# Kernel tuning notes

Hardware: AMD Instinct MI355X
Metric: run time of the kernel (lower is better)

Reference implementation:

```python
import jax, jax.numpy as jnp
import numpy as np

ADAPTER_RATIO = 0.2


def setup_inputs() -> dict:
    key = jax.random.key(0)
    k1, k2, k3, k4, k5 = jax.random.split(key, 5)
    B, C, H, D = 16384, 512, 128, 3  # batch, feature dim, bottleneck, n_domains
    n_text = (D + 1) * 345           # original + 3 domain prompt sets, 345 classes
    return {
        "image_features": jax.random.normal(k1, (B, C), dtype=jnp.float32),
        "domain_label": jax.random.randint(k2, (B,), 0, D),
        "W1": jax.random.normal(k3, (D, C, H), dtype=jnp.float32) * 0.02,
        "W2": jax.random.normal(k4, (D, H, C), dtype=jnp.float32) * 0.02,
        "text_features": jax.random.normal(k5, (n_text, C), dtype=jnp.float32),
        "logit_scale": jnp.ones((1,), dtype=jnp.float32) * jnp.log(jnp.float32(100.0)),
    }


def reference(image_features, domain_label, W1, W2, text_features, logit_scale):
    # Per-sample routed adapters: run all D tiny adapters densely, then gather
    # each sample's routed output (equivalent to torch per-sample dispatch loop).
    h = jax.nn.relu(jnp.einsum("bi,dij->dbj", image_features, W1))   # [D,B,H]
    a = jax.nn.relu(jnp.einsum("dbj,djk->dbk", h, W2))                # [D,B,C]
    adapter_features = jnp.take_along_axis(
        a, domain_label[None, :, None], axis=0)[0]                     # [B,C]
    feats = ADAPTER_RATIO * adapter_features + (1.0 - ADAPTER_RATIO) * image_features
    feats = feats / jnp.linalg.norm(feats, axis=-1, keepdims=True)
    # text features are pre-normalized in the original module
    txt = text_features / jnp.linalg.norm(text_features, axis=-1, keepdims=True)
    logits = jnp.exp(logit_scale[0]) * (feats @ txt.T)                 # [B, n_text]
    return logits
```

## Files before the change

kernel.cpp:

```cpp
#include <hip/hip_runtime.h>
#include <math.h>

typedef __bf16 bf16;
typedef __attribute__((ext_vector_type(8))) __bf16 bf16x8;
typedef __attribute__((ext_vector_type(4))) __bf16 bf16x4;
typedef __attribute__((ext_vector_type(4))) float f32x4;

#define MFMA(a, b, c) __builtin_amdgcn_mfma_f32_16x16x32_bf16((a), (b), (c), 0, 0, 0)
#define BARR() __builtin_amdgcn_s_barrier()
#define SFEN() __builtin_amdgcn_sched_barrier(0)
#define WAITV(n) asm volatile("s_waitcnt vmcnt(" #n ")" ::: "memory")
#define LGKM0() asm volatile("s_waitcnt lgkmcnt(0)" ::: "memory")

static constexpr int NB = 16384;
static constexpr int NC = 512;
static constexpr int NH = 128;
static constexpr int ND = 3;
static constexpr int NT = 1380;
static constexpr int NTP = 1408;
static constexpr int NTILE = 131;
static constexpr int NPMAX = NTILE * 128;

__device__ __forceinline__ void gld16(const bf16* g, void* l) {
  __builtin_amdgcn_global_load_lds(
      (const __attribute__((address_space(1))) void*)g,
      (__attribute__((address_space(3))) void*)l, 16, 0, 0);
}

__global__ __launch_bounds__(1024) void k_prep(
    const float* __restrict__ W1, const float* __restrict__ W2,
    const float* __restrict__ txt, const int* __restrict__ lab,
    bf16* __restrict__ W1t, bf16* __restrict__ W2t, bf16* __restrict__ Tbf,
    int* __restrict__ map, int* __restrict__ dmeta)
{
  __shared__ float tl[64][65];
  __shared__ int woff[16][3];
  __shared__ int segbase[4];
  __shared__ int padded[3];
  const int b = blockIdx.x, t = threadIdx.x;

  if (b < 88) {
    const int wv = t >> 6, lane = t & 63;
    const int row = b * 16 + wv;
    bf16x4* dst = (bf16x4*)(Tbf + (size_t)row * NC);
    if (row < NT) {
      const float4* src = (const float4*)(txt + (size_t)row * NC);
      float4 u0 = src[lane * 2], u1 = src[lane * 2 + 1];
      float ssq = u0.x * u0.x + u0.y * u0.y + u0.z * u0.z + u0.w * u0.w +
                  u1.x * u1.x + u1.y * u1.y + u1.z * u1.z + u1.w * u1.w;
      for (int m = 32; m; m >>= 1) ssq += __shfl_xor(ssq, m, 64);
      float inv = 1.0f / sqrtf(ssq);
      bf16x4 o0 = {(bf16)(u0.x * inv), (bf16)(u0.y * inv), (bf16)(u0.z * inv), (bf16)(u0.w * inv)};
      bf16x4 o1 = {(bf16)(u1.x * inv), (bf16)(u1.y * inv), (bf16)(u1.z * inv), (bf16)(u1.w * inv)};
      dst[lane * 2] = o0; dst[lane * 2 + 1] = o1;
    } else {
      bf16x4 z = {(bf16)0.f, (bf16)0.f, (bf16)0.f, (bf16)0.f};
      dst[lane * 2] = z; dst[lane * 2 + 1] = z;
    }
  } else if (b < 136) {
    const int e = b - 88, d = e >> 4, rem = e & 15;
    const int i0 = (rem >> 1) * 64, n0 = (rem & 1) * 64;
    const int rr = t >> 4, c4 = (t & 15) * 4;
    const float* src = W1 + (size_t)d * NC * NH;
    float4 v = *(const float4*)&src[(size_t)(i0 + rr) * NH + n0 + c4];
    tl[rr][c4] = v.x; tl[rr][c4 + 1] = v.y; tl[rr][c4 + 2] = v.z; tl[rr][c4 + 3] = v.w;
    __syncthreads();
    bf16* dst = W1t + (size_t)d * NH * NC;
    bf16x4 o = {(bf16)tl[c4][rr], (bf16)tl[c4 + 1][rr],
                (bf16)tl[c4 + 2][rr], (bf16)tl[c4 + 3][rr]};
    *(bf16x4*)&dst[(size_t)(n0 + rr) * NC + i0 + c4] = o;
  } else if (b < 184) {
    const int e = b - 136, d = e >> 4, rem = e & 15;
    const int j0 = (rem >> 3) * 64, n0 = (rem & 7) * 64;
    const int rr = t >> 4, c4 = (t & 15) * 4;
    const float* src = W2 + (size_t)d * NH * NC;
    float4 v = *(const float4*)&src[(size_t)(j0 + rr) * NC + n0 + c4];
    tl[rr][c4] = v.x; tl[rr][c4 + 1] = v.y; tl[rr][c4 + 2] = v.z; tl[rr][c4 + 3] = v.w;
    __syncthreads();
    bf16* dst = W2t + (size_t)d * NC * NH;
    bf16x4 o = {(bf16)tl[c4][rr], (bf16)tl[c4 + 1][rr],
                (bf16)tl[c4 + 2][rr], (bf16)tl[c4 + 3][rr]};
    *(bf16x4*)&dst[(size_t)(n0 + rr) * NH + j0 + c4] = o;
  } else {
    const int lane = t & 63, wv = t >> 6;
    int c[3] = {0, 0, 0};
    int ld[16];
    const int base = t * 16;
#pragma unroll
    for (int i = 0; i < 16; ++i) { ld[i] = lab[base + i]; c[ld[i]]++; }
    int exc[3];
#pragma unroll
    for (int d = 0; d < 3; ++d) {
      int v = c[d];
      for (int off = 1; off < 64; off <<= 1) {
        int u = __shfl_up(v, off, 64);
        if (lane >= off) v += u;
      }
      exc[d] = v - c[d];
      if (lane == 63) woff[wv][d] = v;
    }
    __syncthreads();
    if (t == 0) {
      int tot[3] = {0, 0, 0};
      for (int w = 0; w < 16; ++w)
        for (int d = 0; d < 3; ++d) { int v = woff[w][d]; woff[w][d] = tot[d]; tot[d] += v; }
      int s = 0;
      for (int d = 0; d < 3; ++d) {
        padded[d] = (tot[d] + 127) & ~127;
        segbase[d] = s; s += padded[d];
      }
      segbase[3] = s;
      dmeta[NTILE] = s;
    }
    __syncthreads();
    for (int tile = t; tile < NTILE; tile += 1024) {
      const int slot = tile * 128;
      int dd = -1;
      for (int d = 0; d < 3; ++d)
        if (slot >= segbase[d] && slot < segbase[d] + padded[d]) dd = d;
      dmeta[tile] = dd;
    }
    for (int i = t; i < NPMAX; i += 1024) map[i] = -1;
    __syncthreads();
    int pos[3];
#pragma unroll
    for (int d = 0; d < 3; ++d) pos[d] = segbase[d] + woff[wv][d] + exc[d];
#pragma unroll
    for (int i = 0; i < 16; ++i) { int d = ld[i]; map[pos[d]++] = base + i; }
  }
}

__global__ __launch_bounds__(512) void k_adapter(
    const float* __restrict__ X, const bf16* __restrict__ W1t,
    const bf16* __restrict__ W2t, const int* __restrict__ map,
    const int* __restrict__ dmeta, bf16* __restrict__ Fbf)
{
  __shared__ bf16 As[8][64 * 64];
  __shared__ bf16 Hs[64 * 128];
  __shared__ float rssq[8][64];
  __shared__ int smap[64];
  const int bx = blockIdx.x;
  const int d = dmeta[bx >> 1];
  if (d < 0) return;
  const int t = threadIdx.x, w = t >> 6, l = t & 63;
  const int lr = l & 15, lg = l >> 4;
  const int row0 = bx * 64;
  if (t < 64) smap[t] = map[row0 + t];

  int arow = map[row0 + (t >> 3)]; if (arow < 0) arow = 0;
  const float4* Xr = (const float4*)(X + (size_t)arow * NC);
  const int f4b = (t & 7) * 2;
  const int wrow = t >> 3;
  const int wcb = ((t & 7) * 16) ^ ((wrow & 7) << 4);

  float4 R0a, R0b, R1a, R1b;
#define LOADR0(kt) { R0a = Xr[(kt) * 16 + f4b]; R0b = Xr[(kt) * 16 + f4b + 1]; }
#define LOADR1(kt) { R1a = Xr[(kt) * 16 + f4b]; R1b = Xr[(kt) * 16 + f4b + 1]; }
#define CVTW(kt, Ra, Rb) {                                                    \
    bf16x8 v_;                                                                \
    v_[0] = (bf16)Ra.x; v_[1] = (bf16)Ra.y; v_[2] = (bf16)Ra.z;               \
    v_[3] = (bf16)Ra.w; v_[4] = (bf16)Rb.x; v_[5] = (bf16)Rb.y;               \
    v_[6] = (bf16)Rb.z; v_[7] = (bf16)Rb.w;                                   \
    *(bf16x8*)((char*)As[kt] + wrow * 128 + wcb) = v_; }

  f32x4 acc1[4] = {};
  const bf16* W1B = W1t + (size_t)d * NH * NC + (size_t)(w * 16 + lr) * NC;
  LOADR0(0); LOADR1(1);
  CVTW(0, R0a, R0b);
  LOADR0(2);
  LGKM0(); BARR(); SFEN();
#pragma unroll 1
  for (int kt = 0; kt < 8; ++kt) {
    if (kt + 1 < 8) {
      if ((kt & 1) == 0) { CVTW(kt + 1, R1a, R1b); if (kt + 3 < 8) LOADR1(kt + 3); }
      else              { CVTW(kt + 1, R0a, R0b); if (kt + 3 < 8) LOADR0(kt + 3); }
    }
#pragma unroll
    for (int h = 0; h < 2; ++h) {
      bf16x8 a[4];
#pragma unroll
      for (int m = 0; m < 4; ++m) {
        const int r = m * 16 + lr;
        a[m] = *(const bf16x8*)((const char*)As[kt] +
                                r * 128 + ((h * 64 + lg * 16) ^ ((r & 7) << 4)));
      }
      const bf16x8 bq = *(const bf16x8*)(W1B + kt * 64 + h * 32 + lg * 8);
#pragma unroll
      for (int m = 0; m < 4; ++m) acc1[m] = MFMA(a[m], bq, acc1[m]);
    }
    LGKM0(); SFEN(); BARR(); SFEN();
  }
#undef LOADR0
#undef LOADR1
#undef CVTW

#pragma unroll
  for (int m = 0; m < 4; ++m)
#pragma unroll
    for (int r = 0; r < 4; ++r) {
      const int row = m * 16 + lg * 4 + r;
      const int colb = (w * 16 + lr) * 2;
      const float v = acc1[m][r];
      *(bf16*)((char*)Hs + row * 256 + (colb ^ ((row & 7) << 4))) =
          (bf16)(v > 0.f ? v : 0.f);
    }
  __syncthreads();

  f32x4 acc[4][4] = {};
  const bf16* W2B = W2t + (size_t)d * NC * NH + (size_t)(w * 64) * NH;
#pragma unroll
  for (int ks = 0; ks < 4; ++ks) {
    bf16x8 a[4], bq[4];
#pragma unroll
    for (int m = 0; m < 4; ++m) {
      const int r = m * 16 + lr;
      a[m] = *(const bf16x8*)((const char*)Hs +
                              r * 256 + ((ks * 64 + lg * 16) ^ ((r & 7) << 4)));
    }
#pragma unroll
    for (int n = 0; n < 4; ++n)
      bq[n] = *(const bf16x8*)(W2B + (size_t)(n * 16 + lr) * NH + ks * 32 + lg * 8);
#pragma unroll
    for (int m = 0; m < 4; ++m)
#pragma unroll
      for (int n = 0; n < 4; ++n)
        acc[m][n] = MFMA(a[m], bq[n], acc[m][n]);
  }

  const int col0 = w * 64;
#pragma unroll
  for (int m = 0; m < 4; ++m)
#pragma unroll
    for (int r = 0; r < 4; ++r) {
      const int rl = m * 16 + lg * 4 + r;
      const int grow = smap[rl];
      float part = 0.f;
#pragma unroll
      for (int n = 0; n < 4; ++n) {
        const int cw = n * 16 + lr;
        const float xv = (float)*(const bf16*)((const char*)As[w] +
                              rl * 128 + ((cw * 2) ^ ((rl & 7) << 4)));
        float v = acc[m][n][r];
        v = v > 0.f ? v : 0.f;
        v = 0.2f * v + 0.8f * xv;
        acc[m][n][r] = v;
        part += v * v;
      }
      part += __shfl_xor(part, 1, 64);
      part += __shfl_xor(part, 2, 64);
      part += __shfl_xor(part, 4, 64);
      part += __shfl_xor(part, 8, 64);
      if (lr == 0) rssq[w][rl] = part;
      (void)grow;
    }
  __syncthreads();
#pragma unroll
  for (int m = 0; m < 4; ++m)
#pragma unroll
    for (int r = 0; r < 4; ++r) {
      const int rl = m * 16 + lg * 4 + r;
      const int grow = smap[rl];
      if (grow < 0) continue;
      float tot = 0.f;
#pragma unroll
      for (int ww = 0; ww < 8; ++ww) tot += rssq[ww][rl];
      const float inv = 1.0f / sqrtf(tot);
#pragma unroll
      for (int n = 0; n < 4; ++n) {
        const int col = col0 + n * 16 + lr;
        Fbf[(size_t)grow * NC + col] = (bf16)(acc[m][n][r] * inv);
      }
    }
}

__global__ __launch_bounds__(256) void k_gemm3(
    const bf16* __restrict__ Fbf, const bf16* __restrict__ Tbf,
    const float* __restrict__ lsc, float* __restrict__ out)
{
  __shared__ bf16 As[2][128 * 32];
  __shared__ bf16 Bs[2][128 * 32];
  const int bx = blockIdx.x, by = blockIdx.y;
  const int t = threadIdx.x, w = t >> 6, l = t & 63;
  const int wr = w >> 1, wc = w & 1;
  const int lr = l & 15, lg = l >> 4;
  const int row0 = bx * 128, col0 = by * 128;
  const bf16* Ag = Fbf + (size_t)row0 * NC;
  const bf16* Bg = Tbf + (size_t)col0 * NC;

#define STG3(buf, kt)                                                         \
  {                                                                           \
    _Pragma("unroll")                                                         \
    for (int i = 0; i < 2; ++i) {                                             \
      const int off = (i * 256 + t) * 16;                                     \
      const int row = off >> 6;                                               \
      const int src = (off & 63) ^ (((row >> 1) & 3) << 4);                   \
      const size_t go = (size_t)row * NC + (size_t)(kt) * 32 + (src >> 1);    \
      gld16(Ag + go, (char*)As[buf] + off);                                   \
      gld16(Bg + go, (char*)Bs[buf] + off);                                   \
    }                                                                         \
  }

  f32x4 acc[4][4] = {};
  STG3(0, 0);
#pragma unroll 1
  for (int ks = 0; ks < 16; ++ks) {
    const int cur = ks & 1;
    __syncthreads();
    if (ks + 1 < 16) STG3(cur ^ 1, ks + 1);
    bf16x8 a[4], b[4];
#pragma unroll
    for (int m = 0; m < 4; ++m) {
      const int r = wr * 64 + m * 16 + lr;
      a[m] = *(const bf16x8*)&As[cur][r * 32 + ((lg * 8) ^ (((r >> 1) & 3) << 3))];
    }
#pragma unroll
    for (int n = 0; n < 4; ++n) {
      const int r = wc * 64 + n * 16 + lr;
      b[n] = *(const bf16x8*)&Bs[cur][r * 32 + ((lg * 8) ^ (((r >> 1) & 3) << 3))];
    }
#pragma unroll
    for (int m = 0; m < 4; ++m)
#pragma unroll
      for (int n = 0; n < 4; ++n)
        acc[m][n] = MFMA(a[m], b[n], acc[m][n]);
  }

  const float s = expf(lsc[0]);
#pragma unroll
  for (int m = 0; m < 4; ++m)
#pragma unroll
    for (int n = 0; n < 4; ++n)
#pragma unroll
      for (int r = 0; r < 4; ++r) {
        const int row = row0 + wr * 64 + m * 16 + lg * 4 + r;
        const int col = col0 + wc * 64 + n * 16 + lr;
        if (col < NT) out[(size_t)row * NT + col] = s * acc[m][n][r];
      }
#undef STG3
}

extern "C" void kernel_launch(void* const* d_in, const int* in_sizes, int n_in,
                              void* d_out, int out_size, void* d_ws, size_t ws_size,
                              hipStream_t stream) {
  const float* X   = (const float*)d_in[0];
  const int*   lab = (const int*)d_in[1];
  const float* W1  = (const float*)d_in[2];
  const float* W2  = (const float*)d_in[3];
  const float* txt = (const float*)d_in[4];
  const float* lsc = (const float*)d_in[5];
  float* out = (float*)d_out;

  char* ws = (char*)d_ws;
  constexpr size_t SZ_W1T = (size_t)ND * NH * NC * 2;
  constexpr size_t SZ_W2T = (size_t)ND * NC * NH * 2;
  constexpr size_t SZ_TBF = (size_t)NTP * NC * 2;
  constexpr size_t SZ_FBF = (size_t)NB * NC * 2;
  constexpr size_t SZ_MAP = (size_t)NPMAX * 4;
  bf16* W1t = (bf16*)(ws);
  bf16* W2t = (bf16*)(ws + SZ_W1T);
  bf16* Tbf = (bf16*)(ws + SZ_W1T + SZ_W2T);
  bf16* Fbf = (bf16*)(ws + SZ_W1T + SZ_W2T + SZ_TBF);
  int*  map = (int*)(ws + SZ_W1T + SZ_W2T + SZ_TBF + SZ_FBF);
  int*  dmeta = (int*)(ws + SZ_W1T + SZ_W2T + SZ_TBF + SZ_FBF + SZ_MAP);

  k_prep<<<185, 1024, 0, stream>>>(W1, W2, txt, lab, W1t, W2t, Tbf, map, dmeta);
  k_adapter<<<2 * NTILE, 512, 0, stream>>>(X, W1t, W2t, map, dmeta, Fbf);
  k_gemm3<<<dim3(NB / 128, NTP / 128), 256, 0, stream>>>(Fbf, Tbf, lsc, out);
}
```

Before: 99.50 us.

## Shrink adapter tiles to 32 rows with double-buffered LDS and fp32 residual

Result: faster. 97.00 us (-2.5%).

```diff
diff --git a/kernel.cpp b/kernel.cpp
--- a/kernel.cpp
+++ b/kernel.cpp
@@ -130,22 +130,22 @@
   }
 }
 
-__global__ __launch_bounds__(512) void k_adapter(
+__global__ __launch_bounds__(256) void k_adapter(
     const float* __restrict__ X, const bf16* __restrict__ W1t,
     const bf16* __restrict__ W2t, const int* __restrict__ map,
     const int* __restrict__ dmeta, bf16* __restrict__ Fbf)
 {
-  __shared__ bf16 As[8][64 * 64];
-  __shared__ bf16 Hs[64 * 128];
-  __shared__ float rssq[8][64];
-  __shared__ int smap[64];
+  __shared__ bf16 As[2][32 * 64];
+  __shared__ bf16 Hs[32 * 128];
+  __shared__ float rssq[4][32];
+  __shared__ int smap[32];
   const int bx = blockIdx.x;
-  const int d = dmeta[bx >> 1];
+  const int d = dmeta[bx >> 2];
   if (d < 0) return;
   const int t = threadIdx.x, w = t >> 6, l = t & 63;
   const int lr = l & 15, lg = l >> 4;
-  const int row0 = bx * 64;
-  if (t < 64) smap[t] = map[row0 + t];
+  const int row0 = bx * 32;
+  if (t < 32) smap[t] = map[row0 + t];
 
   int arow = map[row0 + (t >> 3)]; if (arow < 0) arow = 0;
   const float4* Xr = (const float4*)(X + (size_t)arow * NC);
@@ -156,37 +156,44 @@
   float4 R0a, R0b, R1a, R1b;
 #define LOADR0(kt) { R0a = Xr[(kt) * 16 + f4b]; R0b = Xr[(kt) * 16 + f4b + 1]; }
 #define LOADR1(kt) { R1a = Xr[(kt) * 16 + f4b]; R1b = Xr[(kt) * 16 + f4b + 1]; }
-#define CVTW(kt, Ra, Rb) {                                                    \
+#define CVTW(buf, Ra, Rb) {                                                   \
     bf16x8 v_;                                                                \
     v_[0] = (bf16)Ra.x; v_[1] = (bf16)Ra.y; v_[2] = (bf16)Ra.z;               \
     v_[3] = (bf16)Ra.w; v_[4] = (bf16)Rb.x; v_[5] = (bf16)Rb.y;               \
     v_[6] = (bf16)Rb.z; v_[7] = (bf16)Rb.w;                                   \
-    *(bf16x8*)((char*)As[kt] + wrow * 128 + wcb) = v_; }
-
-  f32x4 acc1[4] = {};
-  const bf16* W1B = W1t + (size_t)d * NH * NC + (size_t)(w * 16 + lr) * NC;
+    *(bf16x8*)((char*)As[buf] + wrow * 128 + wcb) = v_; }
+
+  f32x4 acc1[2][2] = {};
+  const bf16* W1B = W1t + (size_t)d * NH * NC;
   LOADR0(0); LOADR1(1);
   CVTW(0, R0a, R0b);
   LOADR0(2);
   LGKM0(); BARR(); SFEN();
 #pragma unroll 1
   for (int kt = 0; kt < 8; ++kt) {
+    const int cur = kt & 1;
     if (kt + 1 < 8) {
-      if ((kt & 1) == 0) { CVTW(kt + 1, R1a, R1b); if (kt + 3 < 8) LOADR1(kt + 3); }
-      else              { CVTW(kt + 1, R0a, R0b); if (kt + 3 < 8) LOADR0(kt + 3); }
+      if (cur == 0) { CVTW(1, R1a, R1b); if (kt + 3 < 8) LOADR1(kt + 3); }
+      else          { CVTW(0, R0a, R0b); if (kt + 3 < 8) LOADR0(kt + 3); }
     }
 #pragma unroll
     for (int h = 0; h < 2; ++h) {
-      bf16x8 a[4];
-#pragma unroll
-      for (int m = 0; m < 4; ++m) {
+      bf16x8 a[2], bq[2];
+#pragma unroll
+      for (int m = 0; m < 2; ++m) {
         const int r = m * 16 + lr;
-        a[m] = *(const bf16x8*)((const char*)As[kt] +
+        a[m] = *(const bf16x8*)((const char*)As[cur] +
                                 r * 128 + ((h * 64 + lg * 16) ^ ((r & 7) << 4)));
       }
-      const bf16x8 bq = *(const bf16x8*)(W1B + kt * 64 + h * 32 + lg * 8);
-#pragma unroll
-      for (int m = 0; m < 4; ++m) acc1[m] = MFMA(a[m], bq, acc1[m]);
+#pragma unroll
+      for (int n = 0; n < 2; ++n)
+        bq[n] = *(const bf16x8*)(W1B + (size_t)(w * 32 + n * 16 + lr) * NC +
+                                 kt * 64 + h * 32 + lg * 8);
+#pragma unroll
+      for (int m = 0; m < 2; ++m)
+#pragma unroll
+        for (int n = 0; n < 2; ++n)
+          acc1[m][n] = MFMA(a[m], bq[n], acc1[m][n]);
     }
     LGKM0(); SFEN(); BARR(); SFEN();
   }
@@ -195,54 +202,55 @@
 #undef CVTW
 
 #pragma unroll
-  for (int m = 0; m < 4; ++m)
-#pragma unroll
-    for (int r = 0; r < 4; ++r) {
-      const int row = m * 16 + lg * 4 + r;
-      const int colb = (w * 16 + lr) * 2;
-      const float v = acc1[m][r];
-      *(bf16*)((char*)Hs + row * 256 + (colb ^ ((row & 7) << 4))) =
-          (bf16)(v > 0.f ? v : 0.f);
-    }
+  for (int m = 0; m < 2; ++m)
+#pragma unroll
+    for (int n = 0; n < 2; ++n)
+#pragma unroll
+      for (int r = 0; r < 4; ++r) {
+        const int row = m * 16 + lg * 4 + r;
+        const int colb = (w * 32 + n * 16 + lr) * 2;
+        const float v = acc1[m][n][r];
+        *(bf16*)((char*)Hs + row * 256 + (colb ^ ((row & 7) << 4))) =
+            (bf16)(v > 0.f ? v : 0.f);
+      }
   __syncthreads();
 
-  f32x4 acc[4][4] = {};
-  const bf16* W2B = W2t + (size_t)d * NC * NH + (size_t)(w * 64) * NH;
+  f32x4 acc[2][8] = {};
+  const bf16* W2B = W2t + (size_t)d * NC * NH + (size_t)(w * 128) * NH;
 #pragma unroll
   for (int ks = 0; ks < 4; ++ks) {
-    bf16x8 a[4], bq[4];
-#pragma unroll
-    for (int m = 0; m < 4; ++m) {
+    bf16x8 a[2], bq[8];
+#pragma unroll
+    for (int m = 0; m < 2; ++m) {
       const int r = m * 16 + lr;
       a[m] = *(const bf16x8*)((const char*)Hs +
                               r * 256 + ((ks * 64 + lg * 16) ^ ((r & 7) << 4)));
     }
 #pragma unroll
-    for (int n = 0; n < 4; ++n)
+    for (int n = 0; n < 8; ++n)
       bq[n] = *(const bf16x8*)(W2B + (size_t)(n * 16 + lr) * NH + ks * 32 + lg * 8);
 #pragma unroll
-    for (int m = 0; m < 4; ++m)
-#pragma unroll
-      for (int n = 0; n < 4; ++n)
+    for (int m = 0; m < 2; ++m)
+#pragma unroll
+      for (int n = 0; n < 8; ++n)
         acc[m][n] = MFMA(a[m], bq[n], acc[m][n]);
   }
 
-  const int col0 = w * 64;
-#pragma unroll
-  for (int m = 0; m < 4; ++m)
+  const int col0 = w * 128;
+#pragma unroll
+  for (int m = 0; m < 2; ++m)
 #pragma unroll
     for (int r = 0; r < 4; ++r) {
       const int rl = m * 16 + lg * 4 + r;
       const int grow = smap[rl];
+      const size_t row = grow < 0 ? 0 : (size_t)grow;
       float part = 0.f;
 #pragma unroll
-      for (int n = 0; n < 4; ++n) {
-        const int cw = n * 16 + lr;
-        const float xv = (float)*(const bf16*)((const char*)As[w] +
-                              rl * 128 + ((cw * 2) ^ ((rl & 7) << 4)));
+      for (int n = 0; n < 8; ++n) {
+        const int col = col0 + n * 16 + lr;
         float v = acc[m][n][r];
         v = v > 0.f ? v : 0.f;
-        v = 0.2f * v + 0.8f * xv;
+        v = 0.2f * v + 0.8f * X[row * NC + col];
         acc[m][n][r] = v;
         part += v * v;
       }
@@ -251,11 +259,10 @@
       part += __shfl_xor(part, 4, 64);
       part += __shfl_xor(part, 8, 64);
       if (lr == 0) rssq[w][rl] = part;
-      (void)grow;
     }
   __syncthreads();
 #pragma unroll
-  for (int m = 0; m < 4; ++m)
+  for (int m = 0; m < 2; ++m)
 #pragma unroll
     for (int r = 0; r < 4; ++r) {
       const int rl = m * 16 + lg * 4 + r;
@@ -263,10 +270,10 @@
       if (grow < 0) continue;
       float tot = 0.f;
 #pragma unroll
-      for (int ww = 0; ww < 8; ++ww) tot += rssq[ww][rl];
+      for (int ww = 0; ww < 4; ++ww) tot += rssq[ww][rl];
       const float inv = 1.0f / sqrtf(tot);
 #pragma unroll
-      for (int n = 0; n < 4; ++n) {
+      for (int n = 0; n < 8; ++n) {
         const int col = col0 + n * 16 + lr;
         Fbf[(size_t)grow * NC + col] = (bf16)(acc[m][n][r] * inv);
       }
@@ -364,6 +371,6 @@
   int*  dmeta = (int*)(ws + SZ_W1T + SZ_W2T + SZ_TBF + SZ_FBF + SZ_MAP);
 
   k_prep<<<185, 1024, 0, stream>>>(W1, W2, txt, lab, W1t, W2t, Tbf, map, dmeta);
-  k_adapter<<<2 * NTILE, 512, 0, stream>>>(X, W1t, W2t, map, dmeta, Fbf);
+  k_adapter<<<4 * NTILE, 256, 0, stream>>>(X, W1t, W2t, map, dmeta, Fbf);
   k_gemm3<<<dim3(NB / 128, NTP / 128), 256, 0, stream>>>(Fbf, Tbf, lsc, out);
 }
```

## Shrink adapter X staging to double buffer, preload W1 fragments into registers

Applied to the files above, without the earlier changes.

After: 87.56 us (median of 2 runs). 12.0% less time.

```diff
diff --git a/kernel.cpp b/kernel.cpp
--- a/kernel.cpp
+++ b/kernel.cpp
@@ -135,7 +135,7 @@
     const bf16* __restrict__ W2t, const int* __restrict__ map,
     const int* __restrict__ dmeta, bf16* __restrict__ Fbf)
 {
-  __shared__ bf16 As[8][64 * 64];
+  __shared__ bf16 As[2][64 * 64];
   __shared__ bf16 Hs[64 * 128];
   __shared__ float rssq[8][64];
   __shared__ int smap[64];
@@ -147,6 +147,14 @@
   const int row0 = bx * 64;
   if (t < 64) smap[t] = map[row0 + t];
 
+  const bf16* W1B = W1t + (size_t)d * NH * NC + (size_t)(w * 16 + lr) * NC;
+  bf16x8 w1f[16];
+#pragma unroll
+  for (int kt = 0; kt < 8; ++kt)
+#pragma unroll
+    for (int h = 0; h < 2; ++h)
+      w1f[kt * 2 + h] = *(const bf16x8*)(W1B + kt * 64 + h * 32 + lg * 8);
+
   int arow = map[row0 + (t >> 3)]; if (arow < 0) arow = 0;
   const float4* Xr = (const float4*)(X + (size_t)arow * NC);
   const int f4b = (t & 7) * 2;
@@ -156,24 +164,24 @@
   float4 R0a, R0b, R1a, R1b;
 #define LOADR0(kt) { R0a = Xr[(kt) * 16 + f4b]; R0b = Xr[(kt) * 16 + f4b + 1]; }
 #define LOADR1(kt) { R1a = Xr[(kt) * 16 + f4b]; R1b = Xr[(kt) * 16 + f4b + 1]; }
-#define CVTW(kt, Ra, Rb) {                                                    \
+#define CVTW(buf, Ra, Rb) {                                                   \
     bf16x8 v_;                                                                \
     v_[0] = (bf16)Ra.x; v_[1] = (bf16)Ra.y; v_[2] = (bf16)Ra.z;               \
     v_[3] = (bf16)Ra.w; v_[4] = (bf16)Rb.x; v_[5] = (bf16)Rb.y;               \
     v_[6] = (bf16)Rb.z; v_[7] = (bf16)Rb.w;                                   \
-    *(bf16x8*)((char*)As[kt] + wrow * 128 + wcb) = v_; }
+    *(bf16x8*)((char*)As[buf] + wrow * 128 + wcb) = v_; }
 
   f32x4 acc1[4] = {};
-  const bf16* W1B = W1t + (size_t)d * NH * NC + (size_t)(w * 16 + lr) * NC;
   LOADR0(0); LOADR1(1);
   CVTW(0, R0a, R0b);
   LOADR0(2);
   LGKM0(); BARR(); SFEN();
-#pragma unroll 1
+#pragma unroll
   for (int kt = 0; kt < 8; ++kt) {
+    const int cur = kt & 1;
     if (kt + 1 < 8) {
-      if ((kt & 1) == 0) { CVTW(kt + 1, R1a, R1b); if (kt + 3 < 8) LOADR1(kt + 3); }
-      else              { CVTW(kt + 1, R0a, R0b); if (kt + 3 < 8) LOADR0(kt + 3); }
+      if (cur == 0) { CVTW(1, R1a, R1b); if (kt + 3 < 8) LOADR1(kt + 3); }
+      else          { CVTW(0, R0a, R0b); if (kt + 3 < 8) LOADR0(kt + 3); }
     }
 #pragma unroll
     for (int h = 0; h < 2; ++h) {
@@ -181,12 +189,11 @@
 #pragma unroll
       for (int m = 0; m < 4; ++m) {
         const int r = m * 16 + lr;
-        a[m] = *(const bf16x8*)((const char*)As[kt] +
+        a[m] = *(const bf16x8*)((const char*)As[cur] +
                                 r * 128 + ((h * 64 + lg * 16) ^ ((r & 7) << 4)));
       }
-      const bf16x8 bq = *(const bf16x8*)(W1B + kt * 64 + h * 32 + lg * 8);
-#pragma unroll
-      for (int m = 0; m < 4; ++m) acc1[m] = MFMA(a[m], bq, acc1[m]);
+#pragma unroll
+      for (int m = 0; m < 4; ++m) acc1[m] = MFMA(a[m], w1f[kt * 2 + h], acc1[m]);
     }
     LGKM0(); SFEN(); BARR(); SFEN();
   }
@@ -234,15 +241,14 @@
     for (int r = 0; r < 4; ++r) {
       const int rl = m * 16 + lg * 4 + r;
       const int grow = smap[rl];
+      const size_t row = grow < 0 ? 0 : (size_t)grow;
       float part = 0.f;
 #pragma unroll
       for (int n = 0; n < 4; ++n) {
-        const int cw = n * 16 + lr;
-        const float xv = (float)*(const bf16*)((const char*)As[w] +
-                              rl * 128 + ((cw * 2) ^ ((rl & 7) << 4)));
+        const int col = col0 + n * 16 + lr;
         float v = acc[m][n][r];
         v = v > 0.f ? v : 0.f;
-        v = 0.2f * v + 0.8f * xv;
+        v = 0.2f * v + 0.8f * X[row * NC + col];
         acc[m][n][r] = v;
         part += v * v;
       }
@@ -251,7 +257,6 @@
       part += __shfl_xor(part, 4, 64);
       part += __shfl_xor(part, 8, 64);
       if (lr == 0) rssq[w][rl] = part;
-      (void)grow;
     }
   __syncthreads();
 #pragma unroll
```
